# Performance work log

Hardware: AMD Instinct MI355X
Metric: run time of the kernel (lower is better)

## Reference

```python
import jax, jax.numpy as jnp
import numpy as np

IN_CH = 1
C = 128      # residual_channels
S = 128      # skip_channels
NUM_BLOCKS = 2
NUM_LAYERS = 10
DILATIONS = [2 ** d for _ in range(NUM_BLOCKS) for d in range(NUM_LAYERS)]  # len 20
L = len(DILATIONS)
B = 2
T = 8192


def setup_inputs() -> dict:
    key = jax.random.key(0)
    ks = jax.random.split(key, 12)
    sc = 0.1
    x = jax.random.normal(ks[0], (B, IN_CH, T), dtype=jnp.float32)
    w_in = jax.random.normal(ks[1], (C, IN_CH), dtype=jnp.float32) * sc
    b_in = jax.random.normal(ks[2], (C,), dtype=jnp.float32) * sc
    w_dil = jax.random.normal(ks[3], (L, C, C, 2), dtype=jnp.float32) * sc
    b_dil = jax.random.normal(ks[4], (L, C), dtype=jnp.float32) * sc
    w_tanh = jax.random.normal(ks[5], (L, C, C), dtype=jnp.float32) * sc
    b_tanh = jax.random.normal(ks[6], (L, C), dtype=jnp.float32) * sc
    w_sig = jax.random.normal(ks[7], (L, C, C), dtype=jnp.float32) * sc
    b_sig = jax.random.normal(ks[8], (L, C), dtype=jnp.float32) * sc
    w_skip = jax.random.normal(ks[9], (L, S, C), dtype=jnp.float32) * sc
    b_skip = jax.random.normal(ks[10], (L, S), dtype=jnp.float32) * sc
    return {"x": x, "w_in": w_in, "b_in": b_in, "w_dil": w_dil, "b_dil": b_dil,
            "w_tanh": w_tanh, "b_tanh": b_tanh, "w_sig": w_sig, "b_sig": b_sig,
            "w_skip": w_skip, "b_skip": b_skip}


def _conv1x1(w, b, x):
    # w: [O, C], x: [B, C, T] -> [B, O, T]
    return jnp.einsum('oc,bct->bot', w, x) + b[None, :, None]


def _dilated_conv_k2(w, b, x, d):
    # causal dilated conv, kernel_size=2: y[t] = w0 @ x[t-d] + w1 @ x[t]
    xp = jnp.pad(x, ((0, 0), (0, 0), (d, 0)))  # left causal pad
    y = (jnp.einsum('oc,bct->bot', w[:, :, 0], xp[:, :, :x.shape[-1]])
         + jnp.einsum('oc,bct->bot', w[:, :, 1], xp[:, :, d:]))
    return y + b[None, :, None]


def reference(x, w_in, b_in, w_dil, b_dil, w_tanh, b_tanh, w_sig, b_sig, w_skip, b_skip):
    h = _conv1x1(w_in, b_in, x)  # [B, C, T]
    outputs = []
    skips = []
    for i, d in enumerate(DILATIONS):
        outputs.append(h)
        x_dil = _dilated_conv_k2(w_dil[i], b_dil[i], h, d)
        x_filt = jnp.tanh(_conv1x1(w_tanh[i], b_tanh[i], x_dil))
        x_gate = jax.nn.sigmoid(_conv1x1(w_sig[i], b_sig[i], x_dil))
        x_h = x_gate * x_filt
        skips.append(_conv1x1(w_skip[i], b_skip[i], x_h))
        h = x_h + x_dil  # note: conv_residual is unused in the original forward
    return (jnp.stack(outputs, axis=0), jnp.stack(skips, axis=0))  # [L,B,C,T], [L,B,S,T]
```

## Files before the change

### kernel.cpp

```cpp
#include <hip/hip_runtime.h>
#include <math.h>


typedef _Float16 half8 __attribute__((ext_vector_type(8)));
typedef float floatx4 __attribute__((ext_vector_type(4)));
typedef float float4a __attribute__((ext_vector_type(4), aligned(4)));

namespace {
constexpr int C  = 128;
constexpr int S_ = 128;
constexpr int T  = 8192;
constexpr int B_ = 2;
constexpr int L_ = 20;
constexpr int NT = 32;
constexpr int NTH = 512;
constexpr int P1 = 264;
constexpr int P2 = 136;
constexpr int DIL[L_] = {1,2,4,8,16,32,64,128,256,512,
                         1,2,4,8,16,32,64,128,256,512};
constexpr int WD_FRAG_L = 8 * 4 * 128;
constexpr int W1_FRAG_L = 4 * 4 * 128;
constexpr int NWD = L_ * WD_FRAG_L;
constexpr int NW1 = L_ * W1_FRAG_L;
}

__device__ __forceinline__ float fast_tanh(float x) { return 1.0f - 2.0f / (__expf(2.0f * x) + 1.0f); }
__device__ __forceinline__ float fast_sig (float x) { return 1.0f / (1.0f + __expf(-x)); }

__global__ __launch_bounds__(256) void prep_w(
    const float* __restrict__ wd, const float* __restrict__ wt,
    const float* __restrict__ wsg, const float* __restrict__ wk,
    _Float16* __restrict__ out)
{
    int fi = blockIdx.x * 256 + threadIdx.x;
    if (fi < NWD) {
        int i  = fi / WD_FRAG_L;
        int r  = fi % WD_FRAG_L;
        int kc = r >> 9;
        int q  = (r >> 7) & 3;
        int row = r & 127;
        int tap = kc >> 2;
        int ci0 = (kc & 3) * 32 + q * 8;
        const float* s = wd + ((size_t)(i * 128 + row) * 128 + ci0) * 2 + tap;
        half8 v;
#pragma unroll
        for (int j = 0; j < 8; ++j) v[j] = (_Float16)s[2 * j];
        *(half8*)(out + (size_t)fi * 8) = v;
        return;
    }
    int fi2 = fi - NWD;
    if (fi2 >= 3 * NW1) return;
    int mtx = fi2 / NW1;
    int r   = fi2 % NW1;
    int i   = r / W1_FRAG_L;
    int rr  = r % W1_FRAG_L;
    int kc  = rr >> 9;
    int q   = (rr >> 7) & 3;
    int row = rr & 127;
    const float* base = (mtx == 0) ? wt : ((mtx == 1) ? wsg : wk);
    const float* s = base + (size_t)(i * 128 + row) * 128 + kc * 32 + q * 8;
    half8 v;
#pragma unroll
    for (int j = 0; j < 8; ++j) v[j] = (_Float16)s[j];
    *(half8*)(out + (size_t)(NWD + fi2) * 8) = v;
}

__global__ __launch_bounds__(256) void in_conv(
    const float* __restrict__ x, const float* __restrict__ w_in,
    const float* __restrict__ b_in, float* __restrict__ h0)
{
    int idx = blockIdx.x * 256 + threadIdx.x;
    int t = idx & (T - 1);
    int c = (idx >> 13) & (C - 1);
    int b = idx >> 20;
    h0[idx] = w_in[c] * x[b * T + t] + b_in[c];
}

__global__ __launch_bounds__(NTH, 4) void layer_k(
    const float* __restrict__ h_in,
    float* __restrict__ h_out,
    float* __restrict__ skip_out,
    const _Float16* __restrict__ wd16, const float* __restrict__ bd,
    const _Float16* __restrict__ wt16, const float* __restrict__ bt,
    const _Float16* __restrict__ ws16, const float* __restrict__ bs,
    const _Float16* __restrict__ wk16, const float* __restrict__ bk,
    int d)
{
    __shared__ _Float16 sh[NT * P1];
    __shared__ _Float16 sx[NT * P2];
    _Float16* sxh = sh;

    const int tid = threadIdx.x;
    const int b   = blockIdx.y;
    const int t0  = blockIdx.x * NT;
    const float* hb = h_in + (size_t)b * C * T;

    for (int f = tid; f < C * (NT / 4); f += NTH) {
        int ci = f >> 3, tq = f & 7;
        float4 v = *(const float4*)&hb[ci * T + t0 + tq * 4];
        _Float16* p = &sh[(tq * 4) * P1 + 128 + ci];
        p[0] = (_Float16)v.x; p[P1] = (_Float16)v.y;
        p[2 * P1] = (_Float16)v.z; p[3 * P1] = (_Float16)v.w;
    }
    for (int f = tid; f < C * (NT / 4); f += NTH) {
        int ci = f >> 3, tq = f & 7;
        int ts = t0 + tq * 4 - d;
        float4 v;
        if (ts >= 0) {
            float4a u = *(const float4a*)&hb[ci * T + ts];
            v = make_float4(u.x, u.y, u.z, u.w);
        } else {
            v.x = 0.f;
            v.y = (ts + 1 >= 0) ? hb[ci * T + ts + 1] : 0.f;
            v.z = (ts + 2 >= 0) ? hb[ci * T + ts + 2] : 0.f;
            v.w = (ts + 3 >= 0) ? hb[ci * T + ts + 3] : 0.f;
        }
        _Float16* p = &sh[(tq * 4) * P1 + ci];
        p[0] = (_Float16)v.x; p[P1] = (_Float16)v.y;
        p[2 * P1] = (_Float16)v.z; p[3 * P1] = (_Float16)v.w;
    }
    __syncthreads();

    const int lane = tid & 63;
    const int wv   = tid >> 6;
    const int m16  = lane & 15;
    const int q    = lane >> 4;
    const int cb   = wv * 16;

    half8 wdf[8];
#pragma unroll
    for (int kc = 0; kc < 8; ++kc)
        wdf[kc] = *(const half8*)(wd16 + (size_t)((kc * 4 + q) * 128 + cb + m16) * 8);
    floatx4 bias_d;
#pragma unroll
    for (int r = 0; r < 4; ++r) bias_d[r] = bd[cb + q * 4 + r];

    floatx4 xdacc[2];
#pragma unroll
    for (int nt = 0; nt < 2; ++nt) {
        const int rt = nt * 16 + m16;
        const _Float16* br = &sh[rt * P1 + q * 8];
        half8 bf[8];
#pragma unroll
        for (int kc = 0; kc < 8; ++kc) bf[kc] = *(const half8*)(br + kc * 32);
        floatx4 acc = bias_d;
#pragma unroll
        for (int kc = 0; kc < 8; ++kc)
            acc = __builtin_amdgcn_mfma_f32_16x16x32_f16(wdf[kc], bf[kc], acc, 0, 0, 0);
        xdacc[nt] = acc;
        _Float16* px = &sx[rt * P2 + cb + q * 4];
#pragma unroll
        for (int r = 0; r < 4; ++r) px[r] = (_Float16)acc[r];
    }
    __syncthreads();

    half8 wtf[4], wsf[4];
#pragma unroll
    for (int kc = 0; kc < 4; ++kc) {
        const size_t off = (size_t)((kc * 4 + q) * 128 + cb + m16) * 8;
        wtf[kc] = *(const half8*)(wt16 + off);
        wsf[kc] = *(const half8*)(ws16 + off);
    }
    floatx4 bias_t, bias_s;
#pragma unroll
    for (int r = 0; r < 4; ++r) {
        bias_t[r] = bt[cb + q * 4 + r];
        bias_s[r] = bs[cb + q * 4 + r];
    }

    float* ho = h_out ? h_out + (size_t)b * C * T : nullptr;
#pragma unroll
    for (int nt = 0; nt < 2; ++nt) {
        const int rt = nt * 16 + m16;
        const _Float16* br = &sx[rt * P2 + q * 8];
        half8 bf[4];
#pragma unroll
        for (int kc = 0; kc < 4; ++kc) bf[kc] = *(const half8*)(br + kc * 32);
        floatx4 at = bias_t, as = bias_s;
#pragma unroll
        for (int kc = 0; kc < 4; ++kc) {
            at = __builtin_amdgcn_mfma_f32_16x16x32_f16(wtf[kc], bf[kc], at, 0, 0, 0);
            as = __builtin_amdgcn_mfma_f32_16x16x32_f16(wsf[kc], bf[kc], as, 0, 0, 0);
        }
        _Float16* pxh = &sxh[rt * P2 + cb + q * 4];
#pragma unroll
        for (int r = 0; r < 4; ++r) {
            float xh = fast_tanh(at[r]) * fast_sig(as[r]);
            pxh[r] = (_Float16)xh;
            if (ho)
                ho[(size_t)(cb + q * 4 + r) * T + t0 + rt] = xh + xdacc[nt][r];
        }
    }
    __syncthreads();

    half8 wkf[4];
#pragma unroll
    for (int kc = 0; kc < 4; ++kc)
        wkf[kc] = *(const half8*)(wk16 + (size_t)((kc * 4 + q) * 128 + cb + m16) * 8);
    floatx4 bias_k;
#pragma unroll
    for (int r = 0; r < 4; ++r) bias_k[r] = bk[cb + q * 4 + r];

    float* so = skip_out + (size_t)b * S_ * T;
#pragma unroll
    for (int nt = 0; nt < 2; ++nt) {
        const int rt = nt * 16 + m16;
        const _Float16* br = &sxh[rt * P2 + q * 8];
        half8 bf[4];
#pragma unroll
        for (int kc = 0; kc < 4; ++kc) bf[kc] = *(const half8*)(br + kc * 32);
        floatx4 ak = bias_k;
#pragma unroll
        for (int kc = 0; kc < 4; ++kc)
            ak = __builtin_amdgcn_mfma_f32_16x16x32_f16(wkf[kc], bf[kc], ak, 0, 0, 0);
#pragma unroll
        for (int r = 0; r < 4; ++r)
            so[(size_t)(cb + q * 4 + r) * T + t0 + rt] = ak[r];
    }
}

extern "C" void kernel_launch(void* const* d_in, const int* in_sizes, int n_in,
                              void* d_out, int out_size, void* d_ws, size_t ws_size,
                              hipStream_t stream)
{
    const float* x      = (const float*)d_in[0];
    const float* w_in   = (const float*)d_in[1];
    const float* b_in   = (const float*)d_in[2];
    const float* w_dil  = (const float*)d_in[3];
    const float* b_dil  = (const float*)d_in[4];
    const float* w_tanh = (const float*)d_in[5];
    const float* b_tanh = (const float*)d_in[6];
    const float* w_sig  = (const float*)d_in[7];
    const float* b_sig  = (const float*)d_in[8];
    const float* w_skip = (const float*)d_in[9];
    const float* b_skip = (const float*)d_in[10];

    float* outs  = (float*)d_out;
    float* skips = outs + (size_t)L_ * B_ * C * T;

    _Float16* w16   = (_Float16*)d_ws;
    _Float16* wd16  = w16;
    _Float16* wt16  = w16 + (size_t)NWD * 8;
    _Float16* wsg16 = wt16 + (size_t)NW1 * 8;
    _Float16* wk16  = wsg16 + (size_t)NW1 * 8;

    const int total_frags = NWD + 3 * NW1;
    prep_w<<<dim3((total_frags + 255) / 256), dim3(256), 0, stream>>>(
        w_dil, w_tanh, w_sig, w_skip, w16);

    in_conv<<<dim3(B_ * C * T / 256), dim3(256), 0, stream>>>(x, w_in, b_in, outs);

    for (int i = 0; i < L_; ++i) {
        const float* h_in  = outs + (size_t)i * B_ * C * T;
        float* h_out = (i + 1 < L_) ? outs + (size_t)(i + 1) * B_ * C * T : nullptr;
        float* sk_o  = skips + (size_t)i * B_ * S_ * T;
        layer_k<<<dim3(T / NT, B_), dim3(NTH), 0, stream>>>(
            h_in, h_out, sk_o,
            wd16  + (size_t)i * WD_FRAG_L * 8, b_dil  + (size_t)i * C,
            wt16  + (size_t)i * W1_FRAG_L * 8, b_tanh + (size_t)i * C,
            wsg16 + (size_t)i * W1_FRAG_L * 8, b_sig  + (size_t)i * C,
            wk16  + (size_t)i * W1_FRAG_L * 8, b_skip + (size_t)i * C,
            DIL[i]);
    }
}
```

Before: 542.6 us.

## Feed layers from fp16 time-major side buffers instead of fp32 channel-major outputs

Each layer now also writes its new hidden state as fp16 in a [B,T,C] ping-pong workspace buffer, and the next layer reads that buffer with contiguous half8 loads straight into shared memory. This replaces the strided fp32 reads, the conversion and the scattered transposed LDS writes. The cost is an extra fp16 store per layer and a second input-conv kernel, and it relies on the workspace being large enough to hold the two extra buffers.

```diff
diff --git a/kernel.cpp b/kernel.cpp
--- a/kernel.cpp
+++ b/kernel.cpp
@@ -3,8 +3,8 @@
 
 
 typedef _Float16 half8 __attribute__((ext_vector_type(8)));
+typedef _Float16 half4v __attribute__((ext_vector_type(4)));
 typedef float floatx4 __attribute__((ext_vector_type(4)));
-typedef float float4a __attribute__((ext_vector_type(4), aligned(4)));
 
 namespace {
 constexpr int C  = 128;
@@ -76,9 +76,30 @@
     h0[idx] = w_in[c] * x[b * T + t] + b_in[c];
 }
 
+__global__ __launch_bounds__(256) void in_conv16(
+    const float* __restrict__ x, const float* __restrict__ w_in,
+    const float* __restrict__ b_in, _Float16* __restrict__ h16)
+{
+    int idx = blockIdx.x * 256 + threadIdx.x;
+    int c0 = (idx & 15) * 8;
+    int t  = (idx >> 4) & (T - 1);
+    int b  = idx >> 17;
+    float xv = x[b * T + t];
+    const float4* wp = (const float4*)(w_in + c0);
+    const float4* bp = (const float4*)(b_in + c0);
+    float4 w0 = wp[0], w1 = wp[1], b0 = bp[0], b1 = bp[1];
+    half8 v;
+    v[0] = (_Float16)(w0.x * xv + b0.x); v[1] = (_Float16)(w0.y * xv + b0.y);
+    v[2] = (_Float16)(w0.z * xv + b0.z); v[3] = (_Float16)(w0.w * xv + b0.w);
+    v[4] = (_Float16)(w1.x * xv + b1.x); v[5] = (_Float16)(w1.y * xv + b1.y);
+    v[6] = (_Float16)(w1.z * xv + b1.z); v[7] = (_Float16)(w1.w * xv + b1.w);
+    *(half8*)(h16 + (size_t)idx * 8) = v;
+}
+
 __global__ __launch_bounds__(NTH, 4) void layer_k(
-    const float* __restrict__ h_in,
+    const _Float16* __restrict__ hws_in,
     float* __restrict__ h_out,
+    _Float16* __restrict__ hws_out,
     float* __restrict__ skip_out,
     const _Float16* __restrict__ wd16, const float* __restrict__ bd,
     const _Float16* __restrict__ wt16, const float* __restrict__ bt,
@@ -86,38 +107,27 @@
     const _Float16* __restrict__ wk16, const float* __restrict__ bk,
     int d)
 {
-    __shared__ _Float16 sh[NT * P1];
-    __shared__ _Float16 sx[NT * P2];
+    __shared__ __align__(16) _Float16 sh[NT * P1];
+    __shared__ __align__(16) _Float16 sx[NT * P2];
     _Float16* sxh = sh;
 
     const int tid = threadIdx.x;
     const int b   = blockIdx.y;
     const int t0  = blockIdx.x * NT;
-    const float* hb = h_in + (size_t)b * C * T;
-
-    for (int f = tid; f < C * (NT / 4); f += NTH) {
-        int ci = f >> 3, tq = f & 7;
-        float4 v = *(const float4*)&hb[ci * T + t0 + tq * 4];
-        _Float16* p = &sh[(tq * 4) * P1 + 128 + ci];
-        p[0] = (_Float16)v.x; p[P1] = (_Float16)v.y;
-        p[2 * P1] = (_Float16)v.z; p[3 * P1] = (_Float16)v.w;
-    }
-    for (int f = tid; f < C * (NT / 4); f += NTH) {
-        int ci = f >> 3, tq = f & 7;
-        int ts = t0 + tq * 4 - d;
-        float4 v;
-        if (ts >= 0) {
-            float4a u = *(const float4a*)&hb[ci * T + ts];
-            v = make_float4(u.x, u.y, u.z, u.w);
-        } else {
-            v.x = 0.f;
-            v.y = (ts + 1 >= 0) ? hb[ci * T + ts + 1] : 0.f;
-            v.z = (ts + 2 >= 0) ? hb[ci * T + ts + 2] : 0.f;
-            v.w = (ts + 3 >= 0) ? hb[ci * T + ts + 3] : 0.f;
-        }
-        _Float16* p = &sh[(tq * 4) * P1 + ci];
-        p[0] = (_Float16)v.x; p[P1] = (_Float16)v.y;
-        p[2 * P1] = (_Float16)v.z; p[3 * P1] = (_Float16)v.w;
+    const _Float16* hw = hws_in + (size_t)b * T * C;
+
+#pragma unroll
+    for (int u = 0; u < 2; ++u) {
+        int f = tid + u * NTH;
+        int chunk = f & 15;
+        int tap   = (f >> 4) & 1;
+        int tt    = f >> 5;
+        int ts    = t0 + tt - (tap ? 0 : d);
+        half8 v;
+#pragma unroll
+        for (int j = 0; j < 8; ++j) v[j] = (_Float16)0.0f;
+        if (ts >= 0) v = *(const half8*)(hw + (size_t)ts * C + chunk * 8);
+        *(half8*)(&sh[tt * P1 + tap * 128 + chunk * 8]) = v;
     }
     __syncthreads();
 
@@ -168,7 +178,8 @@
         bias_s[r] = bs[cb + q * 4 + r];
     }
 
-    float* ho = h_out ? h_out + (size_t)b * C * T : nullptr;
+    float*     ho  = h_out   ? h_out   + (size_t)b * C * T : nullptr;
+    _Float16*  hwo = hws_out ? hws_out + (size_t)b * T * C : nullptr;
 #pragma unroll
     for (int nt = 0; nt < 2; ++nt) {
         const int rt = nt * 16 + m16;
@@ -183,13 +194,18 @@
             as = __builtin_amdgcn_mfma_f32_16x16x32_f16(wsf[kc], bf[kc], as, 0, 0, 0);
         }
         _Float16* pxh = &sxh[rt * P2 + cb + q * 4];
+        half4v hv;
 #pragma unroll
         for (int r = 0; r < 4; ++r) {
             float xh = fast_tanh(at[r]) * fast_sig(as[r]);
             pxh[r] = (_Float16)xh;
+            float hn = xh + xdacc[nt][r];
+            hv[r] = (_Float16)hn;
             if (ho)
-                ho[(size_t)(cb + q * 4 + r) * T + t0 + rt] = xh + xdacc[nt][r];
+                ho[(size_t)(cb + q * 4 + r) * T + t0 + rt] = hn;
         }
+        if (hwo)
+            *(half4v*)(hwo + (size_t)(t0 + rt) * C + cb + q * 4) = hv;
     }
     __syncthreads();
 
@@ -243,19 +259,23 @@
     _Float16* wt16  = w16 + (size_t)NWD * 8;
     _Float16* wsg16 = wt16 + (size_t)NW1 * 8;
     _Float16* wk16  = wsg16 + (size_t)NW1 * 8;
+    _Float16* h16a  = wk16 + (size_t)NW1 * 8;
+    _Float16* h16b  = h16a + (size_t)B_ * T * C;
 
     const int total_frags = NWD + 3 * NW1;
     prep_w<<<dim3((total_frags + 255) / 256), dim3(256), 0, stream>>>(
         w_dil, w_tanh, w_sig, w_skip, w16);
 
     in_conv<<<dim3(B_ * C * T / 256), dim3(256), 0, stream>>>(x, w_in, b_in, outs);
+    in_conv16<<<dim3(B_ * T * C / 8 / 256), dim3(256), 0, stream>>>(x, w_in, b_in, h16a);
 
     for (int i = 0; i < L_; ++i) {
-        const float* h_in  = outs + (size_t)i * B_ * C * T;
+        const _Float16* hw_in = (i & 1) ? h16b : h16a;
+        _Float16* hw_out = (i + 1 < L_) ? ((i & 1) ? h16a : h16b) : nullptr;
         float* h_out = (i + 1 < L_) ? outs + (size_t)(i + 1) * B_ * C * T : nullptr;
         float* sk_o  = skips + (size_t)i * B_ * S_ * T;
         layer_k<<<dim3(T / NT, B_), dim3(NTH), 0, stream>>>(
-            h_in, h_out, sk_o,
+            hw_in, h_out, hw_out, sk_o,
             wd16  + (size_t)i * WD_FRAG_L * 8, b_dil  + (size_t)i * C,
             wt16  + (size_t)i * W1_FRAG_L * 8, b_tanh + (size_t)i * C,
             wsg16 + (size_t)i * W1_FRAG_L * 8, b_sig  + (size_t)i * C,
```

After: 529.2 us. 1.03x faster.
